# Optimization experiments

Measured on AMD Instinct MI355X. Metric: run time of the kernel, lower is better.

Reference implementation:

```python
import jax, jax.numpy as jnp
import numpy as np

B, N, K, C = 16, 2048, 20, 64  # batch, points, neighbors, in_dim
OUT = 64
NEG_SLOPE = 0.2


def bn(x, gamma, beta):
    # inference-mode BatchNorm folded to per-channel affine (channel axis=1)
    shape = (1, -1) + (1,) * (x.ndim - 2)
    return x * gamma.reshape(shape) + beta.reshape(shape)


def setup_inputs() -> dict:
    key = jax.random.key(0)
    ks = jax.random.split(key, 20)
    d = {
        'pos':  jax.random.normal(ks[0], (B, 3, N), jnp.float32),
        'x':    jax.random.normal(ks[1], (B, C, N), jnp.float32),
        'glf':  jax.random.normal(ks[2], (B, C // 2, N, K), jnp.float32),
        'appf': jax.random.normal(ks[3], (B, N, K, 8), jnp.float32),
        # basis_matrix: Conv1d(64,64,1,bias=False)
        'basis_W': jax.random.normal(ks[4], (C, C), jnp.float32) * 0.05,
        # dynamic_kernel: Conv2d(8,16)+BN+ReLU+Conv2d(16,32)
        'dk_W1': jax.random.normal(ks[5], (C // 4, 8), jnp.float32) * 0.1,
        'dk_b1': jnp.zeros((C // 4,), jnp.float32),
        'dk_g1': jnp.ones((C // 4,), jnp.float32),
        'dk_be1': jnp.zeros((C // 4,), jnp.float32),
        'dk_W2': jax.random.normal(ks[6], (C // 2, C // 4), jnp.float32) * 0.1,
        'dk_b2': jnp.zeros((C // 2,), jnp.float32),
        # act: BN(64)+ReLU
        'act_g': jnp.ones((C,), jnp.float32),
        'act_b': jnp.zeros((C,), jnp.float32),
        # feature_fusion: Conv2d(64,32,bias=False)+BN+LeakyReLU+Conv2d(32,64,bias=False)+Sigmoid
        'ff_W1': jax.random.normal(ks[7], (C // 2, C), jnp.float32) * 0.05,
        'ff_g1': jnp.ones((C // 2,), jnp.float32),
        'ff_be1': jnp.zeros((C // 2,), jnp.float32),
        'ff_W2': jax.random.normal(ks[8], (C, C // 2), jnp.float32) * 0.05,
        # edge_conv: Conv2d(128,64,bias=False)+BN+LeakyReLU
        'edge_W': jax.random.normal(ks[9], (OUT, 2 * C), jnp.float32) * 0.05,
        'edge_g': jnp.ones((OUT,), jnp.float32),
        'edge_be': jnp.zeros((OUT,), jnp.float32),
    }
    return d


def reference(pos, x, glf, appf, basis_W, dk_W1, dk_b1, dk_g1, dk_be1,
              dk_W2, dk_b2, act_g, act_b, ff_W1, ff_g1, ff_be1, ff_W2,
              edge_W, edge_g, edge_be):
    b, c, n = x.shape
    k = glf.shape[-1]

    # ---- knn graph build (remove self loop) ----
    xx = jnp.sum(pos * pos, axis=1)                       # [B,N]
    inner = jnp.einsum('bdn,bdm->bnm', pos, pos)          # [B,N,N]
    pd = 2.0 * inner - xx[:, :, None] - xx[:, None, :]    # -||pi-pj||^2
    _, idx = jax.lax.top_k(pd, k + 1)
    idx = idx[:, :, 1:]                                   # [B,N,K]

    # ---- dynamic kernel on APPF: [B,N,K,8] -> [B,8,N,K] -> [B,32,N,K] ----
    a = appf.transpose(0, 3, 1, 2)
    h = jnp.einsum('oc,bcnk->bonk', dk_W1, a) + dk_b1[None, :, None, None]
    h = jax.nn.relu(bn(h, dk_g1, dk_be1))
    appf_feat = jnp.einsum('oc,bcnk->bonk', dk_W2, h) + dk_b2[None, :, None, None]

    # ---- RIF + feature fusion (channel attention) ----
    rif = jnp.concatenate([appf_feat, glf], axis=1)       # [B,64,N,K]
    att = jnp.einsum('oc,bcnk->bonk', ff_W1, rif)
    att = jax.nn.leaky_relu(bn(att, ff_g1, ff_be1), NEG_SLOPE)
    att = jax.nn.sigmoid(jnp.einsum('oc,bcnk->bonk', ff_W2, att))
    rif = rif * att

    # ---- basis transform + neighbor gather (feat_select) ----
    bx = jnp.einsum('oc,bcn->bon', basis_W, x)            # [B,64,N]
    gathered = jnp.take_along_axis(
        bx, idx.reshape(b, 1, n * k), axis=2).reshape(b, c, n, k)
    feat = jax.nn.relu(bn(rif * gathered, act_g, act_b))  # [B,64,N,K]

    # ---- edge conv + max over neighbors ----
    pad_x = jnp.broadcast_to(x[..., None], (b, c, n, k))
    e = jnp.concatenate([feat - pad_x, pad_x], axis=1)    # [B,128,N,K]
    out = jnp.einsum('oc,bcnk->bonk', edge_W, e)
    out = jax.nn.leaky_relu(bn(out, edge_g, edge_be), NEG_SLOPE)
    return out.max(axis=-1)                               # [B,64,N]
```

## Files before the change

### kernel.cpp

```cpp
#include <hip/hip_runtime.h>
#include <math.h>

#define B_   16
#define N_   2048
#define K_   20
#define C_   64
#define OUT_ 64
#define NEG_SLOPE 0.2f

__global__ __launch_bounds__(256, 2)
void knn_kernel(const float* __restrict__ pos, int* __restrict__ idx_out) {
    const int t = threadIdx.x;
    const int wv = t >> 6, l = t & 63;
    const int gid = blockIdx.x * 4 + wv;
    const int b = gid / N_, n = gid % N_;
    const float* pb = pos + (size_t)b * 3 * N_;

    const double qx = (double)pb[n];
    const double qy = (double)pb[N_ + n];
    const double qz = (double)pb[2 * N_ + n];
    const double xxn = qx * qx + qy * qy + qz * qz;

    double d[32];
    const int m0 = l * 32;
#pragma unroll
    for (int j4 = 0; j4 < 8; ++j4) {
        float4 px = *(const float4*)(pb + m0 + 4 * j4);
        float4 py = *(const float4*)(pb + N_ + m0 + 4 * j4);
        float4 pz = *(const float4*)(pb + 2 * N_ + m0 + 4 * j4);
#define DCOMP(JJ, PX, PY, PZ)                                            \
        {   double ddx = (double)(PX), ddy = (double)(PY), ddz = (double)(PZ); \
            double inner = qx * ddx + qy * ddy + qz * ddz;               \
            double xxm   = ddx * ddx + ddy * ddy + ddz * ddz;            \
            d[4 * j4 + JJ] = 2.0 * inner - xxn - xxm; }
        DCOMP(0, px.x, py.x, pz.x)
        DCOMP(1, px.y, py.y, pz.y)
        DCOMP(2, px.z, py.z, pz.z)
        DCOMP(3, px.w, py.w, pz.w)
#undef DCOMP
    }

    unsigned sel = 0u;
    for (int r = 0; r < K_ + 1; ++r) {
        double bk = -INFINITY;
        int bi = 0x7FFFFFFF;
#pragma unroll
        for (int j = 0; j < 32; ++j) {
            bool live = ((sel >> j) & 1u) == 0u;
            if (live && d[j] > bk) { bk = d[j]; bi = m0 + j; }
        }
#pragma unroll
        for (int off = 1; off < 64; off <<= 1) {
            double ok = __shfl_xor(bk, off, 64);
            int    oi = __shfl_xor(bi, off, 64);
            if (ok > bk || (ok == bk && oi < bi)) { bk = ok; bi = oi; }
        }
        if ((bi >> 5) == l) sel |= 1u << (bi & 31);
        if (l == 0 && r > 0) idx_out[(size_t)gid * K_ + (r - 1)] = bi;
    }
}

__global__ __launch_bounds__(256)
void bx_kernel_t(const float* __restrict__ x, const float* __restrict__ W,
                 float* __restrict__ bxT) {
    __shared__ float wS[64 * 65];
    __shared__ float xS[64 * 33];
    const int t = threadIdx.x;
    const int b = blockIdx.y;
    const int n0 = blockIdx.x * 32;

    for (int i = t; i < 64 * 64; i += 256) {
        int r = i >> 6, c = i & 63;
        wS[r * 65 + c] = W[i];
    }
    for (int i = t; i < 64 * 32; i += 256) {
        int c = i >> 5, j = i & 31;
        xS[c * 33 + j] = x[((size_t)b * C_ + c) * N_ + n0 + j];
    }
    __syncthreads();

    const int o = t & 63, j0 = t >> 6;
#pragma unroll 1
    for (int j = j0; j < 32; j += 4) {
        float acc = 0.f;
#pragma unroll
        for (int c = 0; c < 64; ++c)
            acc = fmaf(wS[o * 65 + c], xS[c * 33 + j], acc);
        bxT[((size_t)b * N_ + n0 + j) * 64 + o] = acc;
    }
}

#define WPB 4
#define NPW 4
#define NBLK (WPB * NPW)
#define SLICE 2048

__global__ __launch_bounds__(256, 2)
void fused_kernel(const float* __restrict__ x, const float* __restrict__ glf,
                  const float* __restrict__ appf,
                  const float* __restrict__ dk_W1, const float* __restrict__ dk_b1,
                  const float* __restrict__ dk_g1, const float* __restrict__ dk_be1,
                  const float* __restrict__ dk_W2, const float* __restrict__ dk_b2,
                  const float* __restrict__ act_g, const float* __restrict__ act_b,
                  const float* __restrict__ ff_W1, const float* __restrict__ ff_g1,
                  const float* __restrict__ ff_be1, const float* __restrict__ ff_W2,
                  const float* __restrict__ edge_W, const float* __restrict__ edge_g,
                  const float* __restrict__ edge_be,
                  const float* __restrict__ bxT, const int* __restrict__ idx_ws,
                  float* __restrict__ out) {
    __shared__ float wEdT[128 * 64];
    __shared__ float wF1T[64 * 32];
    __shared__ float wF2T[32 * 64];
    __shared__ float lds[WPB * SLICE];

    const int t = threadIdx.x, wv = t >> 6, l = t & 63;
    float* Wb   = lds + wv * SLICE;
    float* RIF  = Wb;
    float* SCR  = Wb + 1280;
    float* XCOL = Wb + 1920;
    int*   IDX  = (int*)(Wb + 1984);

    for (int i = t; i < 64 * 32; i += 256) {
        int o = i >> 5, c4 = i & 31;
        float4 v = ((const float4*)edge_W)[i];
        wEdT[(4 * c4 + 0) * 64 + o] = v.x;
        wEdT[(4 * c4 + 1) * 64 + o] = v.y;
        wEdT[(4 * c4 + 2) * 64 + o] = v.z;
        wEdT[(4 * c4 + 3) * 64 + o] = v.w;
    }
    for (int i = t; i < 32 * 16; i += 256) {
        int o = i >> 4, c4 = i & 15;
        float4 v = ((const float4*)ff_W1)[i];
        wF1T[(4 * c4 + 0) * 32 + o] = v.x;
        wF1T[(4 * c4 + 1) * 32 + o] = v.y;
        wF1T[(4 * c4 + 2) * 32 + o] = v.z;
        wF1T[(4 * c4 + 3) * 32 + o] = v.w;
    }
    for (int i = t; i < 64 * 8; i += 256) {
        int o = i >> 3, c4 = i & 7;
        float4 v = ((const float4*)ff_W2)[i];
        wF2T[(4 * c4 + 0) * 64 + o] = v.x;
        wF2T[(4 * c4 + 1) * 64 + o] = v.y;
        wF2T[(4 * c4 + 2) * 64 + o] = v.z;
        wF2T[(4 * c4 + 3) * 64 + o] = v.w;
    }
    __syncthreads();

    const int raw  = blockIdx.x;
    const int xcd  = raw & 7;
    const int slot = raw >> 3;
    const int b    = xcd * 2 + (slot >> 7);
    const int nblk = (slot & 127) * NBLK;
    const int nw0  = nblk + wv * NPW;

    const int o16 = l >> 2, o32 = l >> 1;
    const int kq5 = (l & 3) * 5, kh10 = (l & 1) * 10;
    const float bdk1h = dk_b1[o16], gdk1h = dk_g1[o16], bedk1h = dk_be1[o16];
    const float bdk2h = dk_b2[o32];
    const float gff1h = ff_g1[o32], beff1h = ff_be1[o32];
    const float gacth = act_g[l],  bacth = act_b[l];
    const float gedgh = edge_g[l], beedgh = edge_be[l];
    const float4 wd1a = *(const float4*)(dk_W1 + o16 * 8);
    const float4 wd1b = *(const float4*)(dk_W1 + o16 * 8 + 4);
    const float4 wd20 = *(const float4*)(dk_W2 + o32 * 16);
    const float4 wd21 = *(const float4*)(dk_W2 + o32 * 16 + 4);
    const float4 wd22 = *(const float4*)(dk_W2 + o32 * 16 + 8);
    const float4 wd23 = *(const float4*)(dk_W2 + o32 * 16 + 12);
    const float* xrow  = x + ((size_t)b * C_ + l) * N_;
    const float* bxb   = bxT + (size_t)b * N_ * 64;

#pragma unroll 1
    for (int i = 0; i < NPW; ++i) {
        const int n = nw0 + i;

        const float xc = xrow[n];
        XCOL[l] = xc;
        if (l < K_) IDX[l] = idx_ws[((size_t)b * N_ + n) * K_ + l];
        if (l >= 32) {
            const int l2 = l - 32;
            const float4* src = (const float4*)(appf + ((size_t)b * N_ + n) * (K_ * 8));
            *(float4*)(SCR + 4 * l2) = src[l2];
            if (l2 < 8) *(float4*)(SCR + 128 + 4 * l2) = src[32 + l2];
        } else {
            const float* g = glf + (((size_t)b * 32 + l) * N_ + n) * K_;
#pragma unroll
            for (int kc = 0; kc < 5; ++kc) {
                float4 v = *(const float4*)(g + 4 * kc);
                RIF[(4 * kc + 0) * 64 + 32 + l] = v.x;
                RIF[(4 * kc + 1) * 64 + 32 + l] = v.y;
                RIF[(4 * kc + 2) * 64 + 32 + l] = v.z;
                RIF[(4 * kc + 3) * 64 + 32 + l] = v.w;
            }
        }

        float base = 0.f;
#pragma unroll
        for (int c = 0; c < 16; ++c) {
            const float w0 = wEdT[(64 + 4 * c + 0) * 64 + l];
            const float w1 = wEdT[(64 + 4 * c + 1) * 64 + l];
            const float w2 = wEdT[(64 + 4 * c + 2) * 64 + l];
            const float w3 = wEdT[(64 + 4 * c + 3) * 64 + l];
            float4 x4 = *(const float4*)(XCOL + 4 * c);
            base = fmaf(w0, x4.x, base); base = fmaf(w1, x4.y, base);
            base = fmaf(w2, x4.z, base); base = fmaf(w3, x4.w, base);
        }

#pragma unroll
        for (int q = 0; q < 5; ++q) {
            const int k = kq5 + q;
            float4 a0 = *(const float4*)(SCR + k * 8);
            float4 a1 = *(const float4*)(SCR + k * 8 + 4);
            float acc = bdk1h;
            acc = fmaf(wd1a.x, a0.x, acc); acc = fmaf(wd1a.y, a0.y, acc);
            acc = fmaf(wd1a.z, a0.z, acc); acc = fmaf(wd1a.w, a0.w, acc);
            acc = fmaf(wd1b.x, a1.x, acc); acc = fmaf(wd1b.y, a1.y, acc);
            acc = fmaf(wd1b.z, a1.z, acc); acc = fmaf(wd1b.w, a1.w, acc);
            float v = acc * gdk1h + bedk1h;
            SCR[160 + k * 16 + o16] = fmaxf(v, 0.f);
        }

#pragma unroll
        for (int q = 0; q < 10; ++q) {
            const int k = kh10 + q;
            const float* hr = SCR + 160 + k * 16;
            float4 h0 = *(const float4*)(hr);
            float4 h1 = *(const float4*)(hr + 4);
            float4 h2 = *(const float4*)(hr + 8);
            float4 h3 = *(const float4*)(hr + 12);
            float acc = bdk2h;
            acc = fmaf(wd20.x, h0.x, acc); acc = fmaf(wd20.y, h0.y, acc);
            acc = fmaf(wd20.z, h0.z, acc); acc = fmaf(wd20.w, h0.w, acc);
            acc = fmaf(wd21.x, h1.x, acc); acc = fmaf(wd21.y, h1.y, acc);
            acc = fmaf(wd21.z, h1.z, acc); acc = fmaf(wd21.w, h1.w, acc);
            acc = fmaf(wd22.x, h2.x, acc); acc = fmaf(wd22.y, h2.y, acc);
            acc = fmaf(wd22.z, h2.z, acc); acc = fmaf(wd22.w, h2.w, acc);
            acc = fmaf(wd23.x, h3.x, acc); acc = fmaf(wd23.y, h3.y, acc);
            acc = fmaf(wd23.z, h3.z, acc); acc = fmaf(wd23.w, h3.w, acc);
            RIF[k * 64 + o32] = acc;
        }

        {
            float acc[10];
#pragma unroll
            for (int q = 0; q < 10; ++q) acc[q] = 0.f;
#pragma unroll
            for (int c = 0; c < 16; ++c) {
                const float w0 = wF1T[(4 * c + 0) * 32 + o32];
                const float w1 = wF1T[(4 * c + 1) * 32 + o32];
                const float w2 = wF1T[(4 * c + 2) * 32 + o32];
                const float w3 = wF1T[(4 * c + 3) * 32 + o32];
#pragma unroll
                for (int q = 0; q < 10; ++q) {
                    float4 r4 = *(const float4*)(RIF + (kh10 + q) * 64 + 4 * c);
                    acc[q] = fmaf(w0, r4.x, acc[q]);
                    acc[q] = fmaf(w1, r4.y, acc[q]);
                    acc[q] = fmaf(w2, r4.z, acc[q]);
                    acc[q] = fmaf(w3, r4.w, acc[q]);
                }
            }
#pragma unroll
            for (int q = 0; q < 10; ++q) {
                float v = acc[q] * gff1h + beff1h;
                v = (v >= 0.f) ? v : NEG_SLOPE * v;
                SCR[(kh10 + q) * 32 + o32] = v;
            }
        }

        float acc2[20];
#pragma unroll
        for (int k = 0; k < 20; ++k) acc2[k] = 0.f;
#pragma unroll
        for (int c = 0; c < 8; ++c) {
            const float w0 = wF2T[(4 * c + 0) * 64 + l];
            const float w1 = wF2T[(4 * c + 1) * 64 + l];
            const float w2 = wF2T[(4 * c + 2) * 64 + l];
            const float w3 = wF2T[(4 * c + 3) * 64 + l];
#pragma unroll
            for (int k = 0; k < 20; ++k) {
                float4 t4 = *(const float4*)(SCR + k * 32 + 4 * c);
                acc2[k] = fmaf(w0, t4.x, acc2[k]);
                acc2[k] = fmaf(w1, t4.y, acc2[k]);
                acc2[k] = fmaf(w2, t4.z, acc2[k]);
                acc2[k] = fmaf(w3, t4.w, acc2[k]);
            }
        }
#pragma unroll
        for (int k = 0; k < 20; ++k) {
            float a = 1.f / (1.f + expf(-acc2[k]));
            int kidx = IDX[k];
            float gth = bxb[(size_t)kidx * 64 + l];
            float v = RIF[k * 64 + l] * a * gth;
            v = v * gacth + bacth;
            v = fmaxf(v, 0.f) - xc;
            RIF[k * 64 + l] = v;
        }

#pragma unroll
        for (int k = 0; k < 20; ++k) acc2[k] = base;
#pragma unroll
        for (int c = 0; c < 16; ++c) {
            const float w0 = wEdT[(4 * c + 0) * 64 + l];
            const float w1 = wEdT[(4 * c + 1) * 64 + l];
            const float w2 = wEdT[(4 * c + 2) * 64 + l];
            const float w3 = wEdT[(4 * c + 3) * 64 + l];
#pragma unroll
            for (int k = 0; k < 20; ++k) {
                float4 r4 = *(const float4*)(RIF + k * 64 + 4 * c);
                acc2[k] = fmaf(w0, r4.x, acc2[k]);
                acc2[k] = fmaf(w1, r4.y, acc2[k]);
                acc2[k] = fmaf(w2, r4.z, acc2[k]);
                acc2[k] = fmaf(w3, r4.w, acc2[k]);
            }
        }
        float mx = -INFINITY;
#pragma unroll
        for (int k = 0; k < 20; ++k) {
            float v = acc2[k] * gedgh + beedgh;
            v = (v >= 0.f) ? v : NEG_SLOPE * v;
            mx = fmaxf(mx, v);
        }
        out[((size_t)b * OUT_ + l) * N_ + n] = mx;
    }
}

extern "C" void kernel_launch(void* const* d_in, const int* in_sizes, int n_in,
                              void* d_out, int out_size, void* d_ws, size_t ws_size,
                              hipStream_t stream) {
    (void)in_sizes; (void)n_in; (void)out_size; (void)ws_size;
    const float* pos     = (const float*)d_in[0];
    const float* x       = (const float*)d_in[1];
    const float* glf     = (const float*)d_in[2];
    const float* appf    = (const float*)d_in[3];
    const float* basis_W = (const float*)d_in[4];
    const float* dk_W1   = (const float*)d_in[5];
    const float* dk_b1   = (const float*)d_in[6];
    const float* dk_g1   = (const float*)d_in[7];
    const float* dk_be1  = (const float*)d_in[8];
    const float* dk_W2   = (const float*)d_in[9];
    const float* dk_b2   = (const float*)d_in[10];
    const float* act_g   = (const float*)d_in[11];
    const float* act_b   = (const float*)d_in[12];
    const float* ff_W1   = (const float*)d_in[13];
    const float* ff_g1   = (const float*)d_in[14];
    const float* ff_be1  = (const float*)d_in[15];
    const float* ff_W2   = (const float*)d_in[16];
    const float* edge_W  = (const float*)d_in[17];
    const float* edge_g  = (const float*)d_in[18];
    const float* edge_be = (const float*)d_in[19];
    float* out = (float*)d_out;

    int*   idx_ws = (int*)d_ws;
    float* bxT    = (float*)((char*)d_ws + (size_t)B_ * N_ * K_ * sizeof(int));

    hipLaunchKernelGGL(knn_kernel, dim3(B_ * N_ / 4), dim3(256), 0, stream,
                       pos, idx_ws);
    hipLaunchKernelGGL(bx_kernel_t, dim3(N_ / 32, B_), dim3(256), 0, stream,
                       x, basis_W, bxT);
    hipLaunchKernelGGL(fused_kernel, dim3(B_ * (N_ / NBLK)), dim3(256), 0, stream,
                       x, glf, appf, dk_W1, dk_b1, dk_g1, dk_be1, dk_W2, dk_b2,
                       act_g, act_b, ff_W1, ff_g1, ff_be1, ff_W2,
                       edge_W, edge_g, edge_be, bxT, idx_ws, out);
}
```

Before: 1.046 ms.

## Split fused kernel into feature and edge-conv kernels with chunked workspace

Splits the monolithic fused kernel into a feat_kernel that writes per-neighbor features to a global workspace and an edge_kernel that reads them back for the edge conv and max. Both kernels run in batch chunks whose size depends on the available workspace. The x-dependent half of the edge conv is precomputed in the bx kernel as baseT. The intent is to lower LDS and register pressure per kernel to raise occupancy, at the cost of a large extra global write and read of the feature tensor and more kernel launches.

```diff
diff --git a/kernel.cpp b/kernel.cpp
--- a/kernel.cpp
+++ b/kernel.cpp
@@ -7,6 +7,11 @@
 #define C_   64
 #define OUT_ 64
 #define NEG_SLOPE 0.2f
+
+#define IDX_BYTES   ((size_t)B_ * N_ * K_ * sizeof(int))
+#define BXT_BYTES   ((size_t)B_ * N_ * 64 * sizeof(float))
+#define BASET_BYTES ((size_t)B_ * N_ * 64 * sizeof(float))
+#define FEAT_CHUNK_BYTES(CB) ((size_t)(CB) * N_ * 20 * 64 * sizeof(float))
 
 __global__ __launch_bounds__(256, 2)
 void knn_kernel(const float* __restrict__ pos, int* __restrict__ idx_out) {
@@ -61,9 +66,11 @@
 }
 
 __global__ __launch_bounds__(256)
-void bx_kernel_t(const float* __restrict__ x, const float* __restrict__ W,
-                 float* __restrict__ bxT) {
+void bx_base_kernel(const float* __restrict__ x, const float* __restrict__ W,
+                    const float* __restrict__ edgeW,
+                    float* __restrict__ bxT, float* __restrict__ baseT) {
     __shared__ float wS[64 * 65];
+    __shared__ float wE[64 * 65];
     __shared__ float xS[64 * 33];
     const int t = threadIdx.x;
     const int b = blockIdx.y;
@@ -72,6 +79,7 @@
     for (int i = t; i < 64 * 64; i += 256) {
         int r = i >> 6, c = i & 63;
         wS[r * 65 + c] = W[i];
+        wE[r * 65 + c] = edgeW[r * 128 + 64 + c];
     }
     for (int i = t; i < 64 * 32; i += 256) {
         int c = i >> 5, j = i & 31;
@@ -82,52 +90,41 @@
     const int o = t & 63, j0 = t >> 6;
 #pragma unroll 1
     for (int j = j0; j < 32; j += 4) {
-        float acc = 0.f;
-#pragma unroll
-        for (int c = 0; c < 64; ++c)
-            acc = fmaf(wS[o * 65 + c], xS[c * 33 + j], acc);
-        bxT[((size_t)b * N_ + n0 + j) * 64 + o] = acc;
+        float acc = 0.f, acb = 0.f;
+#pragma unroll
+        for (int c = 0; c < 64; ++c) {
+            float xv = xS[c * 33 + j];
+            acc = fmaf(wS[o * 65 + c], xv, acc);
+            acb = fmaf(wE[o * 65 + c], xv, acb);
+        }
+        bxT  [((size_t)b * N_ + n0 + j) * 64 + o] = acc;
+        baseT[((size_t)b * N_ + n0 + j) * 64 + o] = acb;
     }
 }
 
-#define WPB 4
-#define NPW 4
-#define NBLK (WPB * NPW)
 #define SLICE 2048
 
 __global__ __launch_bounds__(256, 2)
-void fused_kernel(const float* __restrict__ x, const float* __restrict__ glf,
-                  const float* __restrict__ appf,
-                  const float* __restrict__ dk_W1, const float* __restrict__ dk_b1,
-                  const float* __restrict__ dk_g1, const float* __restrict__ dk_be1,
-                  const float* __restrict__ dk_W2, const float* __restrict__ dk_b2,
-                  const float* __restrict__ act_g, const float* __restrict__ act_b,
-                  const float* __restrict__ ff_W1, const float* __restrict__ ff_g1,
-                  const float* __restrict__ ff_be1, const float* __restrict__ ff_W2,
-                  const float* __restrict__ edge_W, const float* __restrict__ edge_g,
-                  const float* __restrict__ edge_be,
-                  const float* __restrict__ bxT, const int* __restrict__ idx_ws,
-                  float* __restrict__ out) {
-    __shared__ float wEdT[128 * 64];
+void feat_kernel(const float* __restrict__ x, const float* __restrict__ glf,
+                 const float* __restrict__ appf,
+                 const float* __restrict__ dk_W1, const float* __restrict__ dk_b1,
+                 const float* __restrict__ dk_g1, const float* __restrict__ dk_be1,
+                 const float* __restrict__ dk_W2, const float* __restrict__ dk_b2,
+                 const float* __restrict__ act_g, const float* __restrict__ act_b,
+                 const float* __restrict__ ff_W1, const float* __restrict__ ff_g1,
+                 const float* __restrict__ ff_be1, const float* __restrict__ ff_W2,
+                 const float* __restrict__ bxT, const int* __restrict__ idx_ws,
+                 float* __restrict__ featW, int b0) {
     __shared__ float wF1T[64 * 32];
     __shared__ float wF2T[32 * 64];
-    __shared__ float lds[WPB * SLICE];
+    __shared__ float lds[4 * SLICE];
 
     const int t = threadIdx.x, wv = t >> 6, l = t & 63;
     float* Wb   = lds + wv * SLICE;
     float* RIF  = Wb;
     float* SCR  = Wb + 1280;
-    float* XCOL = Wb + 1920;
-    int*   IDX  = (int*)(Wb + 1984);
-
-    for (int i = t; i < 64 * 32; i += 256) {
-        int o = i >> 5, c4 = i & 31;
-        float4 v = ((const float4*)edge_W)[i];
-        wEdT[(4 * c4 + 0) * 64 + o] = v.x;
-        wEdT[(4 * c4 + 1) * 64 + o] = v.y;
-        wEdT[(4 * c4 + 2) * 64 + o] = v.z;
-        wEdT[(4 * c4 + 3) * 64 + o] = v.w;
-    }
+    int*   IDX  = (int*)(Wb + 1920);
+
     for (int i = t; i < 32 * 16; i += 256) {
         int o = i >> 4, c4 = i & 15;
         float4 v = ((const float4*)ff_W1)[i];
@@ -149,35 +146,34 @@
     const int raw  = blockIdx.x;
     const int xcd  = raw & 7;
     const int slot = raw >> 3;
-    const int b    = xcd * 2 + (slot >> 7);
-    const int nblk = (slot & 127) * NBLK;
-    const int nw0  = nblk + wv * NPW;
+    const int b    = b0 + (slot >> 4);
+    const int nslot= xcd * 16 + (slot & 15);
+    const int nw0  = nslot * 16 + wv * 4;
 
     const int o16 = l >> 2, o32 = l >> 1;
     const int kq5 = (l & 3) * 5, kh10 = (l & 1) * 10;
+    const int l2 = l & 31;
     const float bdk1h = dk_b1[o16], gdk1h = dk_g1[o16], bedk1h = dk_be1[o16];
     const float bdk2h = dk_b2[o32];
     const float gff1h = ff_g1[o32], beff1h = ff_be1[o32];
     const float gacth = act_g[l],  bacth = act_b[l];
-    const float gedgh = edge_g[l], beedgh = edge_be[l];
     const float4 wd1a = *(const float4*)(dk_W1 + o16 * 8);
     const float4 wd1b = *(const float4*)(dk_W1 + o16 * 8 + 4);
     const float4 wd20 = *(const float4*)(dk_W2 + o32 * 16);
     const float4 wd21 = *(const float4*)(dk_W2 + o32 * 16 + 4);
     const float4 wd22 = *(const float4*)(dk_W2 + o32 * 16 + 8);
     const float4 wd23 = *(const float4*)(dk_W2 + o32 * 16 + 12);
-    const float* xrow  = x + ((size_t)b * C_ + l) * N_;
-    const float* bxb   = bxT + (size_t)b * N_ * 64;
+    const float* xrow = x + ((size_t)b * C_ + l) * N_;
+    const float* bxb  = bxT + (size_t)b * N_ * 64;
 
 #pragma unroll 1
-    for (int i = 0; i < NPW; ++i) {
+    for (int i = 0; i < 4; ++i) {
         const int n = nw0 + i;
+        const size_t bnloc = (size_t)(b - b0) * N_ + n;
 
         const float xc = xrow[n];
-        XCOL[l] = xc;
         if (l < K_) IDX[l] = idx_ws[((size_t)b * N_ + n) * K_ + l];
         if (l >= 32) {
-            const int l2 = l - 32;
             const float4* src = (const float4*)(appf + ((size_t)b * N_ + n) * (K_ * 8));
             *(float4*)(SCR + 4 * l2) = src[l2];
             if (l2 < 8) *(float4*)(SCR + 128 + 4 * l2) = src[32 + l2];
@@ -191,18 +187,6 @@
                 RIF[(4 * kc + 2) * 64 + 32 + l] = v.z;
                 RIF[(4 * kc + 3) * 64 + 32 + l] = v.w;
             }
-        }
-
-        float base = 0.f;
-#pragma unroll
-        for (int c = 0; c < 16; ++c) {
-            const float w0 = wEdT[(64 + 4 * c + 0) * 64 + l];
-            const float w1 = wEdT[(64 + 4 * c + 1) * 64 + l];
-            const float w2 = wEdT[(64 + 4 * c + 2) * 64 + l];
-            const float w3 = wEdT[(64 + 4 * c + 3) * 64 + l];
-            float4 x4 = *(const float4*)(XCOL + 4 * c);
-            base = fmaf(w0, x4.x, base); base = fmaf(w1, x4.y, base);
-            base = fmaf(w2, x4.z, base); base = fmaf(w3, x4.w, base);
         }
 
 #pragma unroll
@@ -284,6 +268,7 @@
                 acc2[k] = fmaf(w3, t4.w, acc2[k]);
             }
         }
+        float* fdst = featW + bnloc * (20 * 64);
 #pragma unroll
         for (int k = 0; k < 20; ++k) {
             float a = 1.f / (1.f + expf(-acc2[k]));
@@ -292,9 +277,54 @@
             float v = RIF[k * 64 + l] * a * gth;
             v = v * gacth + bacth;
             v = fmaxf(v, 0.f) - xc;
-            RIF[k * 64 + l] = v;
-        }
-
+            fdst[k * 64 + l] = v;
+        }
+    }
+}
+
+__global__ __launch_bounds__(256, 2)
+void edge_kernel(const float* __restrict__ edge_W, const float* __restrict__ edge_g,
+                 const float* __restrict__ edge_be,
+                 const float* __restrict__ featW, const float* __restrict__ baseT,
+                 float* __restrict__ out, int b0) {
+    __shared__ float wEdT[64 * 64];
+    __shared__ float FSs[4 * 1280];
+
+    const int t = threadIdx.x, wv = t >> 6, l = t & 63;
+    float* FS = FSs + wv * 1280;
+
+    for (int i = t; i < 64 * 16; i += 256) {
+        int o = i >> 4, c4 = i & 15;
+        float4 v = ((const float4*)edge_W)[o * 32 + c4];
+        wEdT[(4 * c4 + 0) * 64 + o] = v.x;
+        wEdT[(4 * c4 + 1) * 64 + o] = v.y;
+        wEdT[(4 * c4 + 2) * 64 + o] = v.z;
+        wEdT[(4 * c4 + 3) * 64 + o] = v.w;
+    }
+    __syncthreads();
+
+    const int raw  = blockIdx.x;
+    const int xcd  = raw & 7;
+    const int slot = raw >> 3;
+    const int b    = b0 + (slot >> 4);
+    const int nslot= xcd * 16 + (slot & 15);
+    const int nw0  = nslot * 16 + wv * 4;
+
+    const float gedgh = edge_g[l], beedgh = edge_be[l];
+
+#pragma unroll 1
+    for (int i = 0; i < 4; ++i) {
+        const int n = nw0 + i;
+        const size_t bnloc = (size_t)(b - b0) * N_ + n;
+
+        const float4* fsrc = (const float4*)(featW + bnloc * 1280);
+#pragma unroll
+        for (int j = 0; j < 5; ++j)
+            *(float4*)(FS + (j * 64 + l) * 4) = fsrc[j * 64 + l];
+
+        const float base = baseT[((size_t)b * N_ + n) * 64 + l];
+
+        float acc2[20];
 #pragma unroll
         for (int k = 0; k < 20; ++k) acc2[k] = base;
 #pragma unroll
@@ -305,7 +335,7 @@
             const float w3 = wEdT[(4 * c + 3) * 64 + l];
 #pragma unroll
             for (int k = 0; k < 20; ++k) {
-                float4 r4 = *(const float4*)(RIF + k * 64 + 4 * c);
+                float4 r4 = *(const float4*)(FS + k * 64 + 4 * c);
                 acc2[k] = fmaf(w0, r4.x, acc2[k]);
                 acc2[k] = fmaf(w1, r4.y, acc2[k]);
                 acc2[k] = fmaf(w2, r4.z, acc2[k]);
@@ -326,7 +356,7 @@
 extern "C" void kernel_launch(void* const* d_in, const int* in_sizes, int n_in,
                               void* d_out, int out_size, void* d_ws, size_t ws_size,
                               hipStream_t stream) {
-    (void)in_sizes; (void)n_in; (void)out_size; (void)ws_size;
+    (void)in_sizes; (void)n_in; (void)out_size;
     const float* pos     = (const float*)d_in[0];
     const float* x       = (const float*)d_in[1];
     const float* glf     = (const float*)d_in[2];
@@ -350,14 +380,23 @@
     float* out = (float*)d_out;
 
     int*   idx_ws = (int*)d_ws;
-    float* bxT    = (float*)((char*)d_ws + (size_t)B_ * N_ * K_ * sizeof(int));
+    float* bxT    = (float*)((char*)d_ws + IDX_BYTES);
+    float* baseT  = (float*)((char*)d_ws + IDX_BYTES + BXT_BYTES);
+    float* featW  = (float*)((char*)d_ws + IDX_BYTES + BXT_BYTES + BASET_BYTES);
+
+    const size_t fixed = IDX_BYTES + BXT_BYTES + BASET_BYTES;
+    const int CB = (ws_size >= fixed + FEAT_CHUNK_BYTES(4)) ? 4 : 1;
 
     hipLaunchKernelGGL(knn_kernel, dim3(B_ * N_ / 4), dim3(256), 0, stream,
                        pos, idx_ws);
-    hipLaunchKernelGGL(bx_kernel_t, dim3(N_ / 32, B_), dim3(256), 0, stream,
-                       x, basis_W, bxT);
-    hipLaunchKernelGGL(fused_kernel, dim3(B_ * (N_ / NBLK)), dim3(256), 0, stream,
-                       x, glf, appf, dk_W1, dk_b1, dk_g1, dk_be1, dk_W2, dk_b2,
-                       act_g, act_b, ff_W1, ff_g1, ff_be1, ff_W2,
-                       edge_W, edge_g, edge_be, bxT, idx_ws, out);
+    hipLaunchKernelGGL(bx_base_kernel, dim3(N_ / 32, B_), dim3(256), 0, stream,
+                       x, basis_W, edge_W, bxT, baseT);
+    for (int b0 = 0; b0 < B_; b0 += CB) {
+        hipLaunchKernelGGL(feat_kernel, dim3(CB * 128), dim3(256), 0, stream,
+                           x, glf, appf, dk_W1, dk_b1, dk_g1, dk_be1,
+                           dk_W2, dk_b2, act_g, act_b, ff_W1, ff_g1, ff_be1,
+                           ff_W2, bxT, idx_ws, featW, b0);
+        hipLaunchKernelGGL(edge_kernel, dim3(CB * 128), dim3(256), 0, stream,
+                           edge_W, edge_g, edge_be, featW, baseT, out, b0);
+    }
 }
```

Measured after the change: 995.7 us. 4.8% less time.
